# Performance work log

Measured on AMD Instinct MI355X. Metric: run time of the kernel, lower is better.

## Reference

```python
import jax, jax.numpy as jnp
import numpy as np

P = 16          # patch_len
EPS = 1e-5      # BatchNorm eps


def _dct_mats(L):
    # torch_dct DCT-II matrices. Do: norm='ortho' (orthonormal). D2: norm=None (2*cos).
    n = np.arange(L)
    C = np.cos(np.pi * (n[None, :] + 0.5) * n[:, None] / L)
    s = np.full(L, np.sqrt(2.0 / L)); s[0] = np.sqrt(1.0 / L)
    Do = (s[:, None] * C).astype(np.float32)
    D2 = (2.0 * C).astype(np.float32)
    S = np.full(L, 1.0 / np.sqrt(2.0 * L)); S[0] = 1.0 / (2.0 * np.sqrt(L))
    return jnp.asarray(Do), jnp.asarray(D2), jnp.asarray(S.astype(np.float32))


def _gelu(t):
    return jax.nn.gelu(t, approximate=False)


def _bn(x, g, b, ch_axis=1):
    # training-mode BatchNorm1d: biased batch stats over all axes except channel
    axes = tuple(i for i in range(x.ndim) if i != ch_axis)
    m = x.mean(axes, keepdims=True)
    v = ((x - m) ** 2).mean(axes, keepdims=True)
    shp = [1] * x.ndim; shp[ch_axis] = x.shape[ch_axis]
    return (x - m) / jnp.sqrt(v + EPS) * g.reshape(shp) + b.reshape(shp)


def _quantile(a, q):
    # torch.quantile default 'linear' interpolation over flattened tensor
    s = jnp.sort(a)
    n = a.shape[0]
    pos = q * (n - 1)
    lo = jnp.clip(jnp.floor(pos).astype(jnp.int32), 0, n - 1)
    hi = jnp.clip(lo + 1, 0, n - 1)
    frac = pos - lo.astype(pos.dtype)
    return s[lo] * (1.0 - frac) + s[hi] * frac


def _topk_freq(x, Do5, wf, bf, g, b, wc, bc):
    # TopKFreq: first 5 ortho-DCT coeffs per var (torch detaches via cpu/numpy round trip)
    low = jax.lax.stop_gradient(jnp.einsum('bdl,kl->bdk', x, Do5))  # [B,D,5]
    att = jnp.einsum('bdk,k->bd', low, wf) + bf                      # conv1d k=5 stride=5
    m = att.mean(); v = ((att - m) ** 2).mean()                      # BatchNorm1d(1)
    att = (att - m) / jnp.sqrt(v + EPS) * g + b
    att = _gelu(att)
    a = jax.nn.sigmoid(att * wc + bc)                                # 1x1 conv + sigmoid
    return a[:, :, None]  # [B,D,1]; att1 == att2 (same conv used twice)


def _forward(x, dctconv_w, dctconv_b, dctnorm_g, dctnorm_b, threshold,
             embed_W, embed_b, linres_W, linres_b, depth1_w, depth1_b,
             depthnorm_g, depthnorm_b, tf_fc_w, tf_fc_b, tf_norm_g, tf_norm_b,
             tf_conv_w, tf_conv_b, mlp_w1, mlp_b1, mlp_w2, mlp_b2,
             mlpnorm_g, mlpnorm_b):
    B, L, D = x.shape
    N = L // P
    Do, D2, S = _dct_mats(L)
    dctconv = lambda t: t * dctconv_w[None, :, None] + dctconv_b[None, :, None]

    xp = x.transpose(0, 2, 1)                      # [B,D,L]
    x_res = dctconv(xp)
    z_dct = xp @ D2.T                              # dct, norm=None

    # adaptive high-freq mask (rows of 0/1 per (b,d))
    energy = (z_dct ** 2).sum(-1)                  # [B,D]
    med = jnp.median(energy, axis=1, keepdims=True)
    ne = energy / (med + 1e-6)
    thr = _quantile(ne.ravel(), threshold[0])
    mask = (ne > thr).astype(x.dtype)[:, :, None]

    z = dctconv(z_dct * mask)
    z = _gelu(z)
    z = _bn(z, dctnorm_g, dctnorm_b)
    z1 = (z * S) @ Do + x_res                      # idct(norm=None)

    # non-overlapping patching (stride == patch_len)
    zp = xp.reshape(B * D, N, P)
    ze = jnp.einsum('bnp,dp->bnd', zp, embed_W) + embed_b    # [BD,N,3P]
    z_res = ze.reshape(B, D, N * 3 * P) @ linres_W.T + linres_b  # [B,D,pred]

    zr = ze.reshape(B * D, N, P, 3)                # depthwise conv k=3 stride=3
    z1r = jnp.einsum('bnpj,nj->bnp', zr, depth1_w) + depth1_b[None, :, None]
    zd = _gelu(_bn(z1r, depthnorm_g, depthnorm_b))
    z2 = zd.reshape(B, D, L)

    tf = lambda t: _topk_freq(t, Do[:5], tf_fc_w, tf_fc_b[0], tf_norm_g[0],
                              tf_norm_b[0], tf_conv_w[0], tf_conv_b[0])
    att = tf(z1 + z2)
    z1 = z1 * att
    z2 = z2 * att
    z = z1 + z2
    z_att = tf(z)
    z = _gelu(_bn(z, dctnorm_g, dctnorm_b))
    inter = _gelu(_bn(dctconv(z), dctnorm_g, dctnorm_b)) * z_att
    z1 = z1 * inter + z2
    z2 = z2 * inter + z1                           # uses updated z1
    z = z1 * z2 + z1 + z2
    z = _gelu(_bn(z, dctnorm_g, dctnorm_b))

    # Mlp: fc1 applied twice (identical), gelu gate, BN over vars channel, fc2
    h = z @ mlp_w1.T + mlp_b1                      # [B,D,pred//2]
    h = _gelu(h) * h
    h = _bn(h, mlpnorm_g, mlpnorm_b)
    z_mlp = h @ mlp_w2.T + mlp_b2 + z_res          # [B,D,pred]
    return z_mlp.transpose(0, 2, 1)                # [B,pred,D]


def setup_inputs():
    key = jax.random.key(0)
    ks = jax.random.split(key, 14)
    B, L, D, PRED = 2048, 512, 7, 96
    N, DM, H = L // P, 3 * P, PRED // 2
    f32 = jnp.float32
    rn = lambda k, shape, s: jax.random.normal(k, shape, dtype=f32) * s
    return {
        'x': jax.random.normal(ks[0], (B, L, D), dtype=f32),
        'dctconv_w': rn(ks[1], (D,), 0.5),
        'dctconv_b': rn(ks[2], (D,), 0.02),
        'dctnorm_g': jnp.ones((D,), f32),
        'dctnorm_b': jnp.zeros((D,), f32),
        'threshold': jax.random.uniform(ks[3], (1,), dtype=f32) * 0.5,
        'embed_W': rn(ks[4], (DM, P), 0.1),
        'embed_b': rn(ks[5], (DM,), 0.02),
        'linres_W': rn(ks[6], (PRED, N * DM), 0.02),
        'linres_b': rn(ks[7], (PRED,), 0.02),
        'depth1_w': rn(ks[8], (N, 3), 0.3),
        'depth1_b': rn(ks[9], (N,), 0.02),
        'depthnorm_g': jnp.ones((N,), f32),
        'depthnorm_b': jnp.zeros((N,), f32),
        'tf_fc_w': rn(ks[10], (5,), 0.3),
        'tf_fc_b': rn(ks[10], (1,), 0.02),
        'tf_norm_g': jnp.ones((1,), f32),
        'tf_norm_b': jnp.zeros((1,), f32),
        'tf_conv_w': rn(ks[11], (1,), 0.5),
        'tf_conv_b': rn(ks[11], (1,), 0.02),
        'mlp_w1': rn(ks[12], (H, L), 0.04),
        'mlp_b1': rn(ks[12], (H,), 0.02),
        'mlp_w2': rn(ks[13], (PRED, H), 0.1),
        'mlp_b2': rn(ks[13], (PRED,), 0.02),
        'mlpnorm_g': jnp.ones((D,), f32),
        'mlpnorm_b': jnp.zeros((D,), f32),
    }


def reference(x, dctconv_w, dctconv_b, dctnorm_g, dctnorm_b, threshold,
              embed_W, embed_b, linres_W, linres_b, depth1_w, depth1_b,
              depthnorm_g, depthnorm_b, tf_fc_w, tf_fc_b, tf_norm_g, tf_norm_b,
              tf_conv_w, tf_conv_b, mlp_w1, mlp_b1, mlp_w2, mlp_b2,
              mlpnorm_g, mlpnorm_b):
    return _forward(x, dctconv_w, dctconv_b, dctnorm_g, dctnorm_b, threshold,
                    embed_W, embed_b, linres_W, linres_b, depth1_w, depth1_b,
                    depthnorm_g, depthnorm_b, tf_fc_w, tf_fc_b, tf_norm_g,
                    tf_norm_b, tf_conv_w, tf_conv_b, mlp_w1, mlp_b1, mlp_w2,
                    mlp_b2, mlpnorm_g, mlpnorm_b)
```

## Files before the change

kernel.cpp:

```cpp
#include <hip/hip_runtime.h>
#include <math.h>

#define BB 2048
#define LL 512
#define DD 7
#define BD 14336

constexpr size_t F_XP   = 0;
constexpr size_t F_ZG   = F_XP  + (size_t)BD*512;
constexpr size_t F_Z1   = F_ZG  + (size_t)BD*512;
constexpr size_t F_CLK  = F_Z1  + (size_t)BD*512;
constexpr size_t F_MKL  = F_CLK + 512*512;
constexpr size_t F_U    = F_MKL + 512*512;
constexpr size_t F_CSUM = F_U + 512;
constexpr size_t F_W2   = F_CSUM + 512;
constexpr size_t F_CST  = F_W2 + 96*512;
constexpr size_t F_V    = F_CST + 96;
constexpr size_t F_C2   = F_V + 32*256;
constexpr size_t F_ZRES = F_C2 + 512;
constexpr size_t F_H2   = F_ZRES + (size_t)BD*96;
constexpr size_t F_EN   = F_H2 + (size_t)BD*48;
constexpr size_t F_NE   = F_EN + BD;
constexpr size_t F_ATT  = F_NE + BD;
constexpr size_t F_A1   = F_ATT + BD;
constexpr size_t F_A2   = F_A1 + BD;
constexpr size_t F_RS   = F_A2 + BD;
constexpr size_t F_RQ   = F_RS + BD;
constexpr size_t F_PS   = F_RQ + BD;
constexpr size_t F_PQ   = F_PS + 1792*32;
constexpr size_t F_BN   = F_PQ + 1792*32;
constexpr size_t F_THR  = F_BN + 256;

typedef __attribute__((ext_vector_type(8))) short bf8;
typedef __attribute__((ext_vector_type(4))) short sh4;
typedef __attribute__((ext_vector_type(4))) float f4;

__device__ __forceinline__ float gelu_f(float x) {
  return 0.5f * x * (1.0f + erff(x * 0.70710678118654752440f));
}
__device__ __forceinline__ float sigm_f(float x) {
  return 1.0f / (1.0f + expf(-x));
}
__device__ __forceinline__ float wred(float v) {
#pragma unroll
  for (int o = 32; o > 0; o >>= 1) v += __shfl_down(v, o);
  return v;
}
__device__ __forceinline__ unsigned bfh_u(float v) {
  unsigned u = __float_as_uint(v);
  return (u + 0x7FFFu + ((u >> 16) & 1u)) >> 16;
}
__device__ __forceinline__ float bf2f(unsigned h) { return __uint_as_float(h << 16); }

__global__ void k_gen_b(ushort* __restrict__ B1H, ushort* __restrict__ B1L,
                        ushort* __restrict__ B2H, ushort* __restrict__ B2L) {
  int c = blockIdx.x;
  for (int r = threadIdx.x; r < 512; r += 256) {
    double c1 = cos(3.14159265358979323846 * (r + 0.5) * c / 512.0);
    float v1 = (float)(2.0 * c1);
    unsigned h = bfh_u(v1);
    B1H[(size_t)c*512 + r] = (ushort)h;
    B1L[(size_t)c*512 + r] = (ushort)bfh_u(v1 - bf2f(h));
    double c2 = cos(3.14159265358979323846 * (c + 0.5) * r / 512.0);
    float v2 = (float)(c2 * (r == 0 ? (1.0/1024.0) : (1.0/512.0)));
    h = bfh_u(v2);
    B2H[(size_t)c*512 + r] = (ushort)h;
    B2L[(size_t)c*512 + r] = (ushort)bfh_u(v2 - bf2f(h));
  }
}

__global__ void k_ucsum2(float* __restrict__ u, float* __restrict__ csum,
                         const float* __restrict__ wf) {
  int l = blockIdx.x*256 + threadIdx.x;
  if (l >= 512) return;
  double th2 = 3.14159265358979323846 * (double)(2*l + 1) / 2048.0;
  double s = (l & 1) ? -1.0 : 1.0;
  double S = 0.5*s/tan(th2) - 0.5;
  csum[l] = (float)(1.0/1024.0 + S/512.0);
  double uu = (double)wf[0] * 45.25483399593904156 / 1024.0;
  for (int k = 1; k < 5; ++k)
    uu += (double)wf[k] * 32.0 * cos(3.14159265358979323846*(l+0.5)*k/512.0) / 512.0;
  u[l] = (float)uu;
}

__global__ __launch_bounds__(256) void k_w2(const float* __restrict__ linW,
    const float* __restrict__ linb, const float* __restrict__ eW, const float* __restrict__ eb,
    ushort* __restrict__ W2H, ushort* __restrict__ W2L, float* __restrict__ cst)
{
  __shared__ float sW[768];
  __shared__ float sb[48];
  __shared__ float rbuf[256];
  int o = blockIdx.x, t = threadIdx.x;
  for (int i = t; i < 768; i += 256) sW[i] = eW[i];
  if (t < 48) sb[t] = eb[t];
  __syncthreads();
  const float* lw = linW + (size_t)o * 1536;
  for (int i = t; i < 512; i += 256) {
    int n = i >> 4, p = i & 15;
    float s = 0.f;
    const float* l2 = lw + n*48;
#pragma unroll 8
    for (int m = 0; m < 48; ++m) s += l2[m] * sW[m*16 + p];
    unsigned hb = bfh_u(s);
    W2H[(size_t)o*512 + i] = (ushort)hb;
    W2L[(size_t)o*512 + i] = (ushort)bfh_u(s - bf2f(hb));
  }
  float c = 0.f;
  for (int i = t; i < 1536; i += 256) c += lw[i] * sb[i % 48];
  rbuf[t] = c; __syncthreads();
  for (int off = 128; off > 0; off >>= 1) { if (t < off) rbuf[t] += rbuf[t+off]; __syncthreads(); }
  if (t == 0) cst[o] = rbuf[0] + linb[o];
}

__global__ void k_splitw(const float* __restrict__ src, ushort* __restrict__ H,
                         ushort* __restrict__ L, int n) {
  int i = blockIdx.x*256 + threadIdx.x;
  if (i < n) {
    float v = src[i];
    unsigned hb = bfh_u(v);
    H[i] = (ushort)hb;
    L[i] = (ushort)bfh_u(v - bf2f(hb));
  }
}

__global__ void k_v(const float* __restrict__ eW, const float* __restrict__ eb,
                    const float* __restrict__ dw, const float* __restrict__ db,
                    float* __restrict__ V, float* __restrict__ c2)
{
  int n = blockIdx.x, t = threadIdx.x;
  int p = t >> 4, q = t & 15;
  float s = 0.f;
#pragma unroll
  for (int j = 0; j < 3; ++j) s += eW[(p*3+j)*16 + q] * dw[n*3+j];
  V[(size_t)n*256 + p*16 + q] = s;
  if (q == 0) {
    float c = 0.f;
#pragma unroll
    for (int j = 0; j < 3; ++j) c += eb[p*3+j] * dw[n*3+j];
    c2[n*16+p] = c + db[n];
  }
}

__global__ __launch_bounds__(256) void k_transpose(const float* __restrict__ x,
                                                   float* __restrict__ xp,
                                                   float* __restrict__ en) {
  __shared__ float s[3584];
  int b = blockIdx.x;
  const float* src = x + (size_t)b*3584;
  for (int c = threadIdx.x; c < 896; c += 256) {
    float4 v = *(const float4*)&src[c*4];
    s[c*4+0]=v.x; s[c*4+1]=v.y; s[c*4+2]=v.z; s[c*4+3]=v.w;
  }
  __syncthreads();
  for (int c = threadIdx.x; c < 896; c += 256) {
    int d = c >> 7, cg = c & 127;
    float4 v;
    v.x = s[(cg*4+0)*7 + d]; v.y = s[(cg*4+1)*7 + d];
    v.z = s[(cg*4+2)*7 + d]; v.w = s[(cg*4+3)*7 + d];
    *(float4*)&xp[((size_t)b*7 + d)*512 + cg*4] = v;
  }
  int t = threadIdx.x;
  if (t < 224) {
    int d = t >> 5, c0 = (t & 31) * 16;
    double ss = 0.0, qq = 0.0;
    for (int l = c0; l < c0 + 16; ++l) {
      double v = s[l*7 + d];
      ss += v; qq += v*v;
    }
#pragma unroll
    for (int o = 16; o > 0; o >>= 1) {
      ss += __shfl_down(ss, o, 32);
      qq += __shfl_down(qq, o, 32);
    }
    if ((t & 31) == 0) en[b*7 + d] = (float)(1024.0*qq + 2.0*ss*ss);
  }
}

template<int MODE>
__global__ __launch_bounds__(512) void k_mfma(
    const float* __restrict__ Af32,
    const ushort* __restrict__ AHg, const ushort* __restrict__ ALg,
    const ushort* __restrict__ BHg, const ushort* __restrict__ BLg,
    float* __restrict__ z1out, ushort* __restrict__ GH, ushort* __restrict__ GL,
    const float* __restrict__ bnac, const float* __restrict__ csum,
    const float* __restrict__ xp,
    const float* __restrict__ cw, const float* __restrict__ cb,
    const float* __restrict__ ne, const float* __restrict__ thr,
    float* __restrict__ rs, float* __restrict__ rq)
{
  __shared__ ushort AhS[64*40], AlS[64*40];
  __shared__ ushort BhS[256*40], BlS[256*40];
  const int t = threadIdx.x;
  const int lane = t & 63, w = t >> 6;
  const int l15 = lane & 15, l4 = lane >> 4;
  const int rg = w & 1, cg = w >> 1;
  const int r0 = blockIdx.x * 64, c0 = blockIdx.y * 256;

  f4 acc[2][4];
#pragma unroll
  for (int i = 0; i < 2; ++i)
#pragma unroll
    for (int j = 0; j < 4; ++j) acc[i][j] = (f4){0.f,0.f,0.f,0.f};

  const int arow = t >> 3, ak0 = (t & 7) * 4;

  for (int kt = 0; kt < 512; kt += 32) {
    if (MODE == 2) {
      const float* src = Af32 + (size_t)(r0+arow)*512 + kt + ak0;
      float4 v0 = *(const float4*)src;
      float va[4] = {v0.x,v0.y,v0.z,v0.w};
      sh4 hv, lv;
#pragma unroll
      for (int j = 0; j < 4; ++j) {
        unsigned hb = bfh_u(va[j]);
        hv[j] = (short)hb;
        lv[j] = (short)bfh_u(va[j] - bf2f(hb));
      }
      *(sh4*)&AhS[arow*40 + ak0] = hv;
      *(sh4*)&AlS[arow*40 + ak0] = lv;
    } else {
      *(sh4*)&AhS[arow*40 + ak0] = *(const sh4*)&AHg[(size_t)(r0+arow)*512 + kt + ak0];
      *(sh4*)&AlS[arow*40 + ak0] = *(const sh4*)&ALg[(size_t)(r0+arow)*512 + kt + ak0];
    }
#pragma unroll
    for (int h = 0; h < 2; ++h) {
      int c = t + h*512;
      int brow = c >> 2, bk0 = (c & 3) * 8;
      *(bf8*)&BhS[brow*40 + bk0] = *(const bf8*)&BHg[(size_t)(c0+brow)*512 + kt + bk0];
      *(bf8*)&BlS[brow*40 + bk0] = *(const bf8*)&BLg[(size_t)(c0+brow)*512 + kt + bk0];
    }
    __syncthreads();
    bf8 ah[2], al[2], bh[4], bl[4];
#pragma unroll
    for (int fr = 0; fr < 2; ++fr) {
      int off = (rg*32 + fr*16 + l15)*40 + l4*8;
      ah[fr] = *(const bf8*)&AhS[off];
      al[fr] = *(const bf8*)&AlS[off];
    }
#pragma unroll
    for (int fc = 0; fc < 4; ++fc) {
      int off = (cg*64 + fc*16 + l15)*40 + l4*8;
      bh[fc] = *(const bf8*)&BhS[off];
      bl[fc] = *(const bf8*)&BlS[off];
    }
#pragma unroll
    for (int fr = 0; fr < 2; ++fr)
#pragma unroll
      for (int fc = 0; fc < 4; ++fc) {
        acc[fr][fc] = __builtin_amdgcn_mfma_f32_16x16x32_bf16(ah[fr], bh[fc], acc[fr][fc], 0, 0, 0);
        acc[fr][fc] = __builtin_amdgcn_mfma_f32_16x16x32_bf16(ah[fr], bl[fc], acc[fr][fc], 0, 0, 0);
        acc[fr][fc] = __builtin_amdgcn_mfma_f32_16x16x32_bf16(al[fr], bh[fc], acc[fr][fc], 0, 0, 0);
      }
    __syncthreads();
  }

  const float thv = (MODE == 2) ? thr[0] : 0.f;
#pragma unroll
  for (int fr = 0; fr < 2; ++fr)
#pragma unroll
    for (int j = 0; j < 4; ++j) {
      const int r = r0 + rg*32 + fr*16 + l4*4 + j;
      const int d = r % 7;
      if (MODE == 1) {
        const float aR = bnac[d], cR = bnac[7+d], wv = cw[d], bvv = cb[d];
#pragma unroll
        for (int fc = 0; fc < 4; ++fc) {
          int col = c0 + cg*64 + fc*16 + l15;
          float val = acc[fr][fc][j];
          z1out[(size_t)r*512 + col] = aR*val + cR*csum[col] + xp[(size_t)r*512 + col]*wv + bvv;
        }
      } else {
        float m = (ne[r] > thv) ? 1.0f : 0.0f;
        float wm = cw[d] * m, bvv = cb[d];
        float s = 0.f, q = 0.f;
#pragma unroll
        for (int fc = 0; fc < 4; ++fc) {
          int col = c0 + cg*64 + fc*16 + l15;
          float g = gelu_f(acc[fr][fc][j]*wm + bvv);
          unsigned hb = bfh_u(g);
          GH[(size_t)r*512 + col] = (ushort)hb;
          GL[(size_t)r*512 + col] = (ushort)bfh_u(g - bf2f(hb));
          s += g; q += g*g;
        }
#pragma unroll
        for (int off = 8; off > 0; off >>= 1) {
          s += __shfl_down(s, off, 16);
          q += __shfl_down(q, off, 16);
        }
        if (l15 == 0) { atomicAdd(&rs[r], s); atomicAdd(&rq[r], q); }
      }
    }
}

template<int NCOLS, int MODE>
__global__ __launch_bounds__(256) void k_mfma_nt(
    const float* __restrict__ Af32,
    const ushort* __restrict__ WH, const ushort* __restrict__ WL,
    const float* __restrict__ bias, float* __restrict__ outp,
    const float* __restrict__ ta, const float* __restrict__ tc,
    float* __restrict__ rs, float* __restrict__ rq)
{
  constexpr int NF = NCOLS / 16;
  __shared__ ushort AhS[64*40], AlS[64*40];
  __shared__ ushort BhS[NCOLS*40], BlS[NCOLS*40];
  const int t = threadIdx.x;
  const int lane = t & 63, w = t >> 6;
  const int l15 = lane & 15, l4 = lane >> 4;
  const int r0 = blockIdx.x * 64;

  f4 acc[NF];
#pragma unroll
  for (int fc = 0; fc < NF; ++fc) acc[fc] = (f4){0.f,0.f,0.f,0.f};

  const int arow = t >> 2, ak0 = (t & 3) * 8;
  float taa = 0.f, tcc = 0.f;
  if (MODE == 1) { int d = (r0 + arow) % 7; taa = ta[d]; tcc = tc[d]; }

  for (int kt = 0; kt < 512; kt += 32) {
    {
      const float* src = Af32 + (size_t)(r0+arow)*512 + kt + ak0;
      float4 v0 = *(const float4*)src;
      float4 v1 = *(const float4*)(src+4);
      float va[8] = {v0.x,v0.y,v0.z,v0.w,v1.x,v1.y,v1.z,v1.w};
      bf8 hv, lv;
#pragma unroll
      for (int j = 0; j < 8; ++j) {
        float x = va[j];
        if (MODE == 1) x = gelu_f(taa*x + tcc);
        unsigned hb = bfh_u(x);
        hv[j] = (short)hb;
        lv[j] = (short)bfh_u(x - bf2f(hb));
      }
      *(bf8*)&AhS[arow*40 + ak0] = hv;
      *(bf8*)&AlS[arow*40 + ak0] = lv;
    }
    for (int c = t; c < NCOLS*4; c += 256) {
      int brow = c >> 2, bk0 = (c & 3) * 8;
      *(bf8*)&BhS[brow*40 + bk0] = *(const bf8*)&WH[(size_t)brow*512 + kt + bk0];
      *(bf8*)&BlS[brow*40 + bk0] = *(const bf8*)&WL[(size_t)brow*512 + kt + bk0];
    }
    __syncthreads();
    bf8 ah, al;
    {
      int off = (w*16 + l15)*40 + l4*8;
      ah = *(const bf8*)&AhS[off];
      al = *(const bf8*)&AlS[off];
    }
#pragma unroll
    for (int fc = 0; fc < NF; ++fc) {
      int off = (fc*16 + l15)*40 + l4*8;
      bf8 bh = *(const bf8*)&BhS[off];
      bf8 bl = *(const bf8*)&BlS[off];
      acc[fc] = __builtin_amdgcn_mfma_f32_16x16x32_bf16(ah, bh, acc[fc], 0, 0, 0);
      acc[fc] = __builtin_amdgcn_mfma_f32_16x16x32_bf16(ah, bl, acc[fc], 0, 0, 0);
      acc[fc] = __builtin_amdgcn_mfma_f32_16x16x32_bf16(al, bh, acc[fc], 0, 0, 0);
    }
    __syncthreads();
  }

#pragma unroll
  for (int j = 0; j < 4; ++j) {
    const int r = r0 + w*16 + l4*4 + j;
    float s = 0.f, q = 0.f;
#pragma unroll
    for (int fc = 0; fc < NF; ++fc) {
      int col = fc*16 + l15;
      float v = acc[fc][j] + bias[col];
      if (MODE == 1) { float g = gelu_f(v); v = g*v; }
      outp[(size_t)r*NCOLS + col] = v;
      if (MODE == 1) { s += v; q += v*v; }
    }
    if (MODE == 1) {
#pragma unroll
      for (int off = 8; off > 0; off >>= 1) {
        s += __shfl_down(s, off, 16);
        q += __shfl_down(q, off, 16);
      }
      if (l15 == 0) { rs[r] = s; rq[r] = q; }
    }
  }
}

__global__ void k_ne(const float* __restrict__ en, float* __restrict__ ne) {
  int b = blockIdx.x*256 + threadIdx.x;
  if (b >= 2048) return;
  float e[7], s7[7];
#pragma unroll
  for (int d = 0; d < 7; ++d) { e[d] = en[b*7+d]; s7[d] = e[d]; }
#pragma unroll
  for (int i = 1; i < 7; ++i) {
    float key = s7[i]; int j = i-1;
    while (j >= 0 && s7[j] > key) { s7[j+1] = s7[j]; --j; }
    s7[j+1] = key;
  }
  float med = s7[3] + 1e-6f;
#pragma unroll
  for (int d = 0; d < 7; ++d) ne[b*7+d] = e[d] / med;
}

__global__ __launch_bounds__(1024) void k_thr(const float* __restrict__ ne,
                                              const float* __restrict__ qp, float* __restrict__ out)
{
  __shared__ unsigned s_part[16][8];
  __shared__ unsigned s_bsel, s_R;
  const int t = threadIdx.x;
  const int lane = t & 63, wv = t >> 6;
  unsigned key[14];
#pragma unroll
  for (int j = 0; j < 14; ++j) key[j] = __float_as_uint(ne[t + j*1024]);

  float q = qp[0];
  float pos = q * 14335.0f;
  int lo = (int)floorf(pos);
  if (lo < 0) lo = 0; if (lo > 14335) lo = 14335;
  int hi = lo + 1; if (hi > 14335) hi = 14335;
  float frac = pos - (float)lo;

  unsigned prefix = 0;
  unsigned R = (unsigned)lo;
#pragma unroll 1
  for (int shift = 28; shift >= 0; shift -= 4) {
    unsigned pb = prefix >> shift;
    unsigned long long accb = 0ull;
#pragma unroll
    for (int j = 0; j < 14; ++j) {
      unsigned diff = (key[j] >> shift) - pb;
      accb += (diff < 16u) ? (1ull << (diff*4)) : 0ull;
    }
    unsigned pk[8];
#pragma unroll
    for (int b = 0; b < 8; ++b) {
      unsigned clo = (unsigned)(accb >> (b*4)) & 15u;
      unsigned chi = (unsigned)(accb >> (b*4+32)) & 15u;
      pk[b] = clo | (chi << 16);
    }
#pragma unroll
    for (int b = 0; b < 8; ++b)
#pragma unroll
      for (int o = 32; o > 0; o >>= 1) pk[b] += __shfl_down(pk[b], o);
    if (lane == 0) {
#pragma unroll
      for (int b = 0; b < 8; ++b) s_part[wv][b] = pk[b];
    }
    __syncthreads();
    if (t == 0) {
      unsigned tot[16];
#pragma unroll
      for (int i = 0; i < 8; ++i) {
        unsigned s = 0;
#pragma unroll
        for (int w2 = 0; w2 < 16; ++w2) s += s_part[w2][i];
        tot[i] = s & 0xFFFFu; tot[i+8] = s >> 16;
      }
      unsigned cum = 0, bsel = 15;
#pragma unroll 1
      for (int b = 0; b < 16; ++b) {
        if (cum + tot[b] > R) { bsel = (unsigned)b; break; }
        cum += tot[b];
      }
      s_bsel = bsel; s_R = R - cum;
    }
    __syncthreads();
    prefix |= (s_bsel << shift);
    R = s_R;
    __syncthreads();
  }
  unsigned cle = 0, mn = 0xFFFFFFFFu;
#pragma unroll
  for (int j = 0; j < 14; ++j) {
    cle += (key[j] <= prefix) ? 1u : 0u;
    if (key[j] > prefix && key[j] < mn) mn = key[j];
  }
#pragma unroll
  for (int o = 32; o > 0; o >>= 1) {
    cle += __shfl_down(cle, o);
    unsigned m2 = __shfl_down(mn, o);
    mn = (m2 < mn) ? m2 : mn;
  }
  if (lane == 0) { s_part[wv][0] = cle; s_part[wv][1] = mn; }
  __syncthreads();
  if (t == 0) {
    unsigned C = 0, M = 0xFFFFFFFFu;
#pragma unroll
    for (int w2 = 0; w2 < 16; ++w2) {
      C += s_part[w2][0];
      if (s_part[w2][1] < M) M = s_part[w2][1];
    }
    unsigned vhiKey = (C > (unsigned)hi) ? prefix : M;
    if (vhiKey == 0xFFFFFFFFu) vhiKey = prefix;
    float vlo = __uint_as_float(prefix);
    float vhi = __uint_as_float(vhiKey);
    out[0] = vlo*(1.0f-frac) + vhi*frac;
  }
}

__global__ __launch_bounds__(256) void k_bnfin_rows(const float* __restrict__ rs,
    const float* __restrict__ rq, int nch, int nrows, double count,
    const float* __restrict__ gamma, const float* __restrict__ beta, float* __restrict__ out)
{
  __shared__ double sd[256];
  int ch = blockIdx.x, t = threadIdx.x;
  double s = 0.0, q = 0.0;
  for (int i = ch + t*nch; i < nrows; i += 256*nch) { s += rs[i]; q += rq[i]; }
  sd[t] = s; __syncthreads();
  for (int o = 128; o > 0; o >>= 1) { if (t < o) sd[t] += sd[t+o]; __syncthreads(); }
  double S = sd[0]; __syncthreads();
  sd[t] = q; __syncthreads();
  for (int o = 128; o > 0; o >>= 1) { if (t < o) sd[t] += sd[t+o]; __syncthreads(); }
  if (t == 0) {
    double m = S / count;
    double v = sd[0] / count - m*m; if (v < 0.0) v = 0.0;
    double inv = 1.0 / sqrt(v + 1e-5);
    out[ch]       = (float)(gamma[ch] * inv);
    out[nch + ch] = (float)(beta[ch] - m * gamma[ch] * inv);
  }
}

__global__ __launch_bounds__(256) void k_bnfin_part(const float* __restrict__ pS,
    const float* __restrict__ pQ, int nparts, int nch, double count,
    const float* __restrict__ gamma, const float* __restrict__ beta, float* __restrict__ out)
{
  __shared__ double sd[256];
  int ch = blockIdx.x, t = threadIdx.x;
  double s = 0.0, q = 0.0;
  for (int i = t; i < nparts; i += 256) { s += pS[(size_t)i*nch + ch]; q += pQ[(size_t)i*nch + ch]; }
  sd[t] = s; __syncthreads();
  for (int o = 128; o > 0; o >>= 1) { if (t < o) sd[t] += sd[t+o]; __syncthreads(); }
  double S = sd[0]; __syncthreads();
  sd[t] = q; __syncthreads();
  for (int o = 128; o > 0; o >>= 1) { if (t < o) sd[t] += sd[t+o]; __syncthreads(); }
  if (t == 0) {
    double m = S / count;
    double v = sd[0] / count - m*m; if (v < 0.0) v = 0.0;
    double inv = 1.0 / sqrt(v + 1e-5);
    out[ch]       = (float)(gamma[ch] * inv);
    out[nch + ch] = (float)(beta[ch] - m * gamma[ch] * inv);
  }
}

__global__ __launch_bounds__(256) void k_patch(const float* __restrict__ xp,
    const float* __restrict__ V, const float* __restrict__ c2,
    float* __restrict__ z1r, float* __restrict__ pS, float* __restrict__ pQ)
{
  __shared__ float sx[8][512];
  __shared__ float aS[32], aQ[32];
  int t = threadIdx.x;
  int r0 = blockIdx.x * 8;
  for (int c = t; c < 1024; c += 256) {
    int row = c >> 7, cg = c & 127;
    *(float4*)&sx[row][cg*4] = *(const float4*)&xp[(size_t)(r0+row)*512 + cg*4];
  }
  if (t < 32) { aS[t] = 0.f; aQ[t] = 0.f; }
  __syncthreads();
  float vreg[2][16]; float cc[2]; int nn_[2], oo[2];
#pragma unroll
  for (int h = 0; h < 2; ++h) {
    int o = t + h*256;
    oo[h] = o;
    int n = o >> 4, p = o & 15;
    nn_[h] = n;
#pragma unroll
    for (int qg = 0; qg < 4; ++qg) {
      float4 v4 = *(const float4*)&V[(size_t)n*256 + p*16 + qg*4];
      vreg[h][qg*4+0]=v4.x; vreg[h][qg*4+1]=v4.y; vreg[h][qg*4+2]=v4.z; vreg[h][qg*4+3]=v4.w;
    }
    cc[h] = c2[o];
  }
  float sum[2] = {0.f,0.f}, sq[2] = {0.f,0.f};
  for (int row = 0; row < 8; ++row) {
#pragma unroll
    for (int h = 0; h < 2; ++h) {
      const float* xr = &sx[row][nn_[h]*16];
      float val = cc[h];
#pragma unroll
      for (int qq = 0; qq < 16; ++qq) val += vreg[h][qq] * xr[qq];
      z1r[(size_t)(r0+row)*512 + oo[h]] = val;
      sum[h] += val; sq[h] += val*val;
    }
  }
#pragma unroll
  for (int h = 0; h < 2; ++h) {
    atomicAdd(&aS[nn_[h]], sum[h]);
    atomicAdd(&aQ[nn_[h]], sq[h]);
  }
  __syncthreads();
  if (t < 32) { pS[(size_t)blockIdx.x*32 + t] = aS[t]; pQ[(size_t)blockIdx.x*32 + t] = aQ[t]; }
}

__global__ void k_att(const float* __restrict__ z1, const float* __restrict__ z1r,
    const float* __restrict__ bn2, const float* __restrict__ u, const float* __restrict__ fcb,
    float* __restrict__ att)
{
  int r = blockIdx.x*4 + (threadIdx.x >> 6);
  int lane = threadIdx.x & 63;
  const float* z1p = z1 + (size_t)r*512;
  const float* zrp = z1r + (size_t)r*512;
  float s = 0.f;
#pragma unroll
  for (int h = 0; h < 2; ++h) {
    int i = lane*4 + h*256;
    int n = i >> 4;
    float a2n = bn2[n], c2n = bn2[32+n];
    float4 zr = *(const float4*)&zrp[i];
    float4 zv = *(const float4*)&z1p[i];
    float4 uv = *(const float4*)&u[i];
    s += (zv.x + gelu_f(a2n*zr.x + c2n)) * uv.x;
    s += (zv.y + gelu_f(a2n*zr.y + c2n)) * uv.y;
    s += (zv.z + gelu_f(a2n*zr.z + c2n)) * uv.z;
    s += (zv.w + gelu_f(a2n*zr.w + c2n)) * uv.w;
  }
  s = wred(s);
  if (lane == 0) att[r] = s + fcb[0];
}

__global__ __launch_bounds__(1024) void k_tf(const float* __restrict__ att,
    const float* __restrict__ pg, const float* __restrict__ pb,
    const float* __restrict__ pwc, const float* __restrict__ pbc,
    const float* __restrict__ pfb, float* __restrict__ a1, float* __restrict__ a2)
{
  __shared__ double sd[1024];
  __shared__ float sh[4];
  const int t = threadIdx.x;
  float g = pg[0], b = pb[0], wc = pwc[0], bc = pbc[0], fb = pfb[0];
  double s = 0.0, q = 0.0;
  for (int i = t; i < BD; i += 1024) { double v = att[i]; s += v; q += v*v; }
  sd[t] = s; __syncthreads();
  for (int o = 512; o > 0; o >>= 1) { if (t < o) sd[t] += sd[t+o]; __syncthreads(); }
  double S1 = sd[0]; __syncthreads();
  sd[t] = q; __syncthreads();
  for (int o = 512; o > 0; o >>= 1) { if (t < o) sd[t] += sd[t+o]; __syncthreads(); }
  if (t == 0) {
    double m = S1 / 14336.0;
    double v = sd[0] / 14336.0 - m*m; if (v < 0.0) v = 0.0;
    sh[0] = (float)m; sh[1] = (float)(1.0 / sqrt(v + 1e-5));
  }
  __syncthreads();
  float m1 = sh[0], i1 = sh[1];
  s = 0.0; q = 0.0;
  for (int i = t; i < BD; i += 1024) {
    float v = att[i];
    float an = (v - m1) * i1 * g + b;
    float av = sigm_f(gelu_f(an) * wc + bc);
    a1[i] = av;
    float t2 = av * (v - fb) + fb;
    s += t2; q += (double)t2 * t2;
  }
  __syncthreads();
  sd[t] = s; __syncthreads();
  for (int o = 512; o > 0; o >>= 1) { if (t < o) sd[t] += sd[t+o]; __syncthreads(); }
  double S2 = sd[0]; __syncthreads();
  sd[t] = q; __syncthreads();
  for (int o = 512; o > 0; o >>= 1) { if (t < o) sd[t] += sd[t+o]; __syncthreads(); }
  if (t == 0) {
    double m = S2 / 14336.0;
    double v = sd[0] / 14336.0 - m*m; if (v < 0.0) v = 0.0;
    sh[2] = (float)m; sh[3] = (float)(1.0 / sqrt(v + 1e-5));
  }
  __syncthreads();
  float m2 = sh[2], i2 = sh[3];
  for (int i = t; i < BD; i += 1024) {
    float t2 = a1[i] * (att[i] - fb) + fb;
    float an = (t2 - m2) * i2 * g + b;
    a2[i] = sigm_f(gelu_f(an) * wc + bc);
  }
}

__global__ void k_statsA(const float* __restrict__ z1, const float* __restrict__ z1r,
    const float* __restrict__ bn2, const float* __restrict__ a1,
    float* __restrict__ rs, float* __restrict__ rq)
{
  int r = blockIdx.x*4 + (threadIdx.x >> 6);
  int lane = threadIdx.x & 63;
  float av = a1[r];
  const float* z1p = z1 + (size_t)r*512;
  const float* zrp = z1r + (size_t)r*512;
  float s = 0.f, q = 0.f;
#pragma unroll
  for (int h = 0; h < 2; ++h) {
    int i = lane*4 + h*256;
    int n = i >> 4;
    float a2n = bn2[n], c2n = bn2[32+n];
    float4 zr = *(const float4*)&zrp[i];
    float4 zv = *(const float4*)&z1p[i];
    float A0 = (zv.x + gelu_f(a2n*zr.x + c2n)) * av;
    float A1 = (zv.y + gelu_f(a2n*zr.y + c2n)) * av;
    float A2 = (zv.z + gelu_f(a2n*zr.z + c2n)) * av;
    float A3 = (zv.w + gelu_f(a2n*zr.w + c2n)) * av;
    s += A0+A1+A2+A3; q += A0*A0+A1*A1+A2*A2+A3*A3;
  }
  s = wred(s); q = wred(q);
  if (lane == 0) { rs[r] = s; rq[r] = q; }
}

__global__ void k_statsC(const float* __restrict__ z1, const float* __restrict__ z1r,
    const float* __restrict__ bn2, const float* __restrict__ a1,
    const float* __restrict__ bn3, const float* __restrict__ cw, const float* __restrict__ cb,
    float* __restrict__ rs, float* __restrict__ rq)
{
  int r = blockIdx.x*4 + (threadIdx.x >> 6);
  int lane = threadIdx.x & 63;
  int d = r % 7;
  float av = a1[r];
  float b3a = bn3[d], b3c = bn3[7+d], wv = cw[d], bv = cb[d];
  const float* z1p = z1 + (size_t)r*512;
  const float* zrp = z1r + (size_t)r*512;
  float s = 0.f, q = 0.f;
#pragma unroll
  for (int h = 0; h < 2; ++h) {
    int i = lane*4 + h*256;
    int n = i >> 4;
    float a2n = bn2[n], c2n = bn2[32+n];
    float4 zr = *(const float4*)&zrp[i];
    float4 zv = *(const float4*)&z1p[i];
#pragma unroll
    for (int e = 0; e < 4; ++e) {
      float ze = (e==0?zr.x:e==1?zr.y:e==2?zr.z:zr.w);
      float z1e = (e==0?zv.x:e==1?zv.y:e==2?zv.z:zv.w);
      float A = (z1e + gelu_f(a2n*ze + c2n)) * av;
      float C = wv*gelu_f(b3a*A + b3c) + bv;
      s += C; q += C*C;
    }
  }
  s = wred(s); q = wred(q);
  if (lane == 0) { rs[r] = s; rq[r] = q; }
}

__global__ void k_final(const float* __restrict__ z1, const float* __restrict__ z1r,
    const float* __restrict__ bn2, const float* __restrict__ a1, const float* __restrict__ a2,
    const float* __restrict__ bn3, const float* __restrict__ bn4,
    const float* __restrict__ cw, const float* __restrict__ cb,
    float* __restrict__ zf, float* __restrict__ rs, float* __restrict__ rq)
{
  int r = blockIdx.x*4 + (threadIdx.x >> 6);
  int lane = threadIdx.x & 63;
  int d = r % 7;
  float av = a1[r], a2v = a2[r];
  float b3a = bn3[d], b3c = bn3[7+d], b4a = bn4[d], b4c = bn4[7+d];
  float wv = cw[d], bv = cb[d];
  const float* z1p = z1 + (size_t)r*512;
  const float* zrp = z1r + (size_t)r*512;
  float* zfp = zf + (size_t)r*512;
  float s = 0.f, q = 0.f;
#pragma unroll
  for (int h = 0; h < 2; ++h) {
    int i = lane*4 + h*256;
    int n = i >> 4;
    float a2n = bn2[n], c2n = bn2[32+n];
    float4 zr = *(const float4*)&zrp[i];
    float4 zv = *(const float4*)&z1p[i];
    float4 ov;
#pragma unroll
    for (int e = 0; e < 4; ++e) {
      float ze = (e==0?zr.x:e==1?zr.y:e==2?zr.z:zr.w);
      float z1e = (e==0?zv.x:e==1?zv.y:e==2?zv.z:zv.w);
      float z1v = z1e * av;
      float z2v = gelu_f(a2n*ze + c2n) * av;
      float A = z1v + z2v;
      float C = wv*gelu_f(b3a*A + b3c) + bv;
      float inter = gelu_f(b4a*C + b4c) * a2v;
      float z1n = z1v*inter + z2v;
      float z2n = z2v*inter + z1n;
      float zfv = z1n*z2n + z1n + z2n;
      (e==0?ov.x:e==1?ov.y:e==2?ov.z:ov.w) = zfv;
      s += zfv; q += zfv*zfv;
    }
    *(float4*)&zfp[i] = ov;
  }
  s = wred(s); q = wred(q);
  if (lane == 0) { rs[r] = s; rq[r] = q; }
}

__global__ __launch_bounds__(256) void k_out(const float* __restrict__ h2,
    const float* __restrict__ bn6, const float* __restrict__ w2, const float* __restrict__ b2,
    const float* __restrict__ zres, float* __restrict__ out)
{
  int idx = blockIdx.x*256 + threadIdx.x;
  int r = idx / 96, o = idx - r*96;
  int d = r % 7, b = r / 7;
  float a6 = bn6[d], c6 = bn6[7+d];
  const float* hp = h2 + (size_t)r*48;
  const float* wp = w2 + o*48;
  float s = 0.f;
#pragma unroll
  for (int j4 = 0; j4 < 12; ++j4) {
    float4 hv = *(const float4*)&hp[j4*4];
    float4 wv = *(const float4*)&wp[j4*4];
    s += (a6*hv.x + c6)*wv.x + (a6*hv.y + c6)*wv.y
       + (a6*hv.z + c6)*wv.z + (a6*hv.w + c6)*wv.w;
  }
  out[(size_t)b*672 + o*7 + d] = s + b2[o] + zres[(size_t)r*96 + o];
}

extern "C" void kernel_launch(void* const* d_in, const int* in_sizes, int n_in,
                              void* d_out, int out_size, void* d_ws, size_t ws_size,
                              hipStream_t stream) {
  const float* x          = (const float*)d_in[0];
  const float* dctconv_w  = (const float*)d_in[1];
  const float* dctconv_b  = (const float*)d_in[2];
  const float* dctnorm_g  = (const float*)d_in[3];
  const float* dctnorm_b  = (const float*)d_in[4];
  const float* threshold  = (const float*)d_in[5];
  const float* embed_W    = (const float*)d_in[6];
  const float* embed_b    = (const float*)d_in[7];
  const float* linres_W   = (const float*)d_in[8];
  const float* linres_b   = (const float*)d_in[9];
  const float* depth1_w   = (const float*)d_in[10];
  const float* depth1_b   = (const float*)d_in[11];
  const float* depthnorm_g= (const float*)d_in[12];
  const float* depthnorm_b= (const float*)d_in[13];
  const float* tf_fc_w    = (const float*)d_in[14];
  const float* tf_fc_b    = (const float*)d_in[15];
  const float* tf_norm_g  = (const float*)d_in[16];
  const float* tf_norm_b  = (const float*)d_in[17];
  const float* tf_conv_w  = (const float*)d_in[18];
  const float* tf_conv_b  = (const float*)d_in[19];
  const float* mlp_w1     = (const float*)d_in[20];
  const float* mlp_b1     = (const float*)d_in[21];
  const float* mlp_w2     = (const float*)d_in[22];
  const float* mlp_b2     = (const float*)d_in[23];
  const float* mlpnorm_g  = (const float*)d_in[24];
  const float* mlpnorm_b  = (const float*)d_in[25];
  float* out = (float*)d_out;
  float* ws  = (float*)d_ws;

  float* XP   = ws + F_XP;
  float* ZG   = ws + F_ZG;
  ushort* ZGH = (ushort*)(ws + F_ZG);
  ushort* ZGL = ZGH + (size_t)BD*512;
  float* Z1   = ws + F_Z1;
  ushort* B1H = (ushort*)(ws + F_CLK);
  ushort* B1L = B1H + 512*512;
  ushort* W2H = (ushort*)(ws + F_CLK + 131072);
  ushort* W2L = W2H + 96*512;
  ushort* W1H = W2L + 96*512;
  ushort* W1L = W1H + 48*512;
  ushort* B2H = (ushort*)(ws + F_MKL);
  ushort* B2L = B2H + 512*512;
  float* U    = ws + F_U;
  float* CSUM = ws + F_CSUM;
  float* CSTp = ws + F_CST;
  float* Vp   = ws + F_V;
  float* C2p  = ws + F_C2;
  float* ZRES = ws + F_ZRES;
  float* H2p  = ws + F_H2;
  float* EN   = ws + F_EN;
  float* NEp  = ws + F_NE;
  float* ATTp = ws + F_ATT;
  float* A1p  = ws + F_A1;
  float* A2p  = ws + F_A2;
  float* RS   = ws + F_RS;
  float* RQ   = ws + F_RQ;
  float* PS   = ws + F_PS;
  float* PQ   = ws + F_PQ;
  float* BN0  = ws + F_BN;
  float* BN2  = ws + F_BN + 16;
  float* BN3  = ws + F_BN + 80;
  float* BN4  = ws + F_BN + 96;
  float* BN5  = ws + F_BN + 112;
  float* BN6  = ws + F_BN + 128;
  float* THRp = ws + F_THR;

  k_gen_b<<<512, 256, 0, stream>>>(B1H, B1L, B2H, B2L);
  k_ucsum2<<<2, 256, 0, stream>>>(U, CSUM, tf_fc_w);
  k_w2<<<96, 256, 0, stream>>>(linres_W, linres_b, embed_W, embed_b, W2H, W2L, CSTp);
  k_splitw<<<96, 256, 0, stream>>>(mlp_w1, W1H, W1L, 48*512);
  k_v<<<32, 256, 0, stream>>>(embed_W, embed_b, depth1_w, depth1_b, Vp, C2p);
  k_transpose<<<2048, 256, 0, stream>>>(x, XP, EN);
  k_ne<<<8, 256, 0, stream>>>(EN, NEp);
  k_thr<<<1, 1024, 0, stream>>>(NEp, threshold, THRp);
  hipMemsetAsync(RS, 0, 2*BD*sizeof(float), stream);
  k_mfma<2><<<dim3(224,2), 512, 0, stream>>>(XP, nullptr, nullptr, B1H, B1L,
      nullptr, ZGH, ZGL, nullptr, nullptr, nullptr, dctconv_w, dctconv_b,
      NEp, THRp, RS, RQ);
  k_bnfin_rows<<<7, 256, 0, stream>>>(RS, RQ, 7, BD, 1048576.0, dctnorm_g, dctnorm_b, BN0);
  k_mfma<1><<<dim3(224,2), 512, 0, stream>>>(nullptr, ZGH, ZGL, B2H, B2L,
      Z1, nullptr, nullptr, BN0, CSUM, XP, dctconv_w, dctconv_b,
      nullptr, nullptr, nullptr, nullptr);
  k_patch<<<1792, 256, 0, stream>>>(XP, Vp, C2p, ZG, PS, PQ);
  k_bnfin_part<<<32, 256, 0, stream>>>(PS, PQ, 1792, 32, 229376.0, depthnorm_g, depthnorm_b, BN2);
  k_mfma_nt<96,0><<<224, 256, 0, stream>>>(XP, W2H, W2L, CSTp, ZRES,
      nullptr, nullptr, nullptr, nullptr);
  k_att<<<3584, 256, 0, stream>>>(Z1, ZG, BN2, U, tf_fc_b, ATTp);
  k_tf<<<1, 1024, 0, stream>>>(ATTp, tf_norm_g, tf_norm_b, tf_conv_w, tf_conv_b, tf_fc_b, A1p, A2p);
  k_statsA<<<3584, 256, 0, stream>>>(Z1, ZG, BN2, A1p, RS, RQ);
  k_bnfin_rows<<<7, 256, 0, stream>>>(RS, RQ, 7, BD, 1048576.0, dctnorm_g, dctnorm_b, BN3);
  k_statsC<<<3584, 256, 0, stream>>>(Z1, ZG, BN2, A1p, BN3, dctconv_w, dctconv_b, RS, RQ);
  k_bnfin_rows<<<7, 256, 0, stream>>>(RS, RQ, 7, BD, 1048576.0, dctnorm_g, dctnorm_b, BN4);
  k_final<<<3584, 256, 0, stream>>>(Z1, ZG, BN2, A1p, A2p, BN3, BN4, dctconv_w, dctconv_b, XP, RS, RQ);
  k_bnfin_rows<<<7, 256, 0, stream>>>(RS, RQ, 7, BD, 1048576.0, dctnorm_g, dctnorm_b, BN5);
  k_mfma_nt<48,1><<<224, 256, 0, stream>>>(XP, W1H, W1L, mlp_b1, H2p,
      BN5, BN5+7, RS, RQ);
  k_bnfin_rows<<<7, 256, 0, stream>>>(RS, RQ, 7, BD, 98304.0, mlpnorm_g, mlpnorm_b, BN6);
  k_out<<<5376, 256, 0, stream>>>(H2p, BN6, mlp_w2, mlp_b2, ZRES, out);
}
```

Before: 379.8 us.

## Fuse setup kernels, retile DCT GEMMs, drop statsA pass, store final z as bf16 split

```diff
diff --git a/kernel.cpp b/kernel.cpp
--- a/kernel.cpp
+++ b/kernel.cpp
@@ -30,6 +30,7 @@
 constexpr size_t F_PQ   = F_PS + 1792*32;
 constexpr size_t F_BN   = F_PQ + 1792*32;
 constexpr size_t F_THR  = F_BN + 256;
+constexpr size_t F_W1   = F_THR + 16;
 
 typedef __attribute__((ext_vector_type(8))) short bf8;
 typedef __attribute__((ext_vector_type(4))) short sh4;
@@ -52,99 +53,99 @@
 }
 __device__ __forceinline__ float bf2f(unsigned h) { return __uint_as_float(h << 16); }
 
-__global__ void k_gen_b(ushort* __restrict__ B1H, ushort* __restrict__ B1L,
-                        ushort* __restrict__ B2H, ushort* __restrict__ B2L) {
-  int c = blockIdx.x;
-  for (int r = threadIdx.x; r < 512; r += 256) {
-    double c1 = cos(3.14159265358979323846 * (r + 0.5) * c / 512.0);
-    float v1 = (float)(2.0 * c1);
-    unsigned h = bfh_u(v1);
-    B1H[(size_t)c*512 + r] = (ushort)h;
-    B1L[(size_t)c*512 + r] = (ushort)bfh_u(v1 - bf2f(h));
-    double c2 = cos(3.14159265358979323846 * (c + 0.5) * r / 512.0);
-    float v2 = (float)(c2 * (r == 0 ? (1.0/1024.0) : (1.0/512.0)));
-    h = bfh_u(v2);
-    B2H[(size_t)c*512 + r] = (ushort)h;
-    B2L[(size_t)c*512 + r] = (ushort)bfh_u(v2 - bf2f(h));
-  }
-}
-
-__global__ void k_ucsum2(float* __restrict__ u, float* __restrict__ csum,
-                         const float* __restrict__ wf) {
-  int l = blockIdx.x*256 + threadIdx.x;
-  if (l >= 512) return;
-  double th2 = 3.14159265358979323846 * (double)(2*l + 1) / 2048.0;
-  double s = (l & 1) ? -1.0 : 1.0;
-  double S = 0.5*s/tan(th2) - 0.5;
-  csum[l] = (float)(1.0/1024.0 + S/512.0);
-  double uu = (double)wf[0] * 45.25483399593904156 / 1024.0;
-  for (int k = 1; k < 5; ++k)
-    uu += (double)wf[k] * 32.0 * cos(3.14159265358979323846*(l+0.5)*k/512.0) / 512.0;
-  u[l] = (float)uu;
-}
-
-__global__ __launch_bounds__(256) void k_w2(const float* __restrict__ linW,
-    const float* __restrict__ linb, const float* __restrict__ eW, const float* __restrict__ eb,
+#define PI1024 0.00306796157577128218f
+
+__global__ __launch_bounds__(256) void k_setup(
+    ushort* __restrict__ B1H, ushort* __restrict__ B1L,
+    ushort* __restrict__ B2H, ushort* __restrict__ B2L,
+    float* __restrict__ u, float* __restrict__ csum, const float* __restrict__ wf,
+    const float* __restrict__ eW, const float* __restrict__ eb,
+    const float* __restrict__ dw, const float* __restrict__ db,
+    float* __restrict__ V, float* __restrict__ c2,
+    const float* __restrict__ mlpw1, ushort* __restrict__ W1H, ushort* __restrict__ W1L,
+    const float* __restrict__ linW, const float* __restrict__ linb,
     ushort* __restrict__ W2H, ushort* __restrict__ W2L, float* __restrict__ cst)
 {
   __shared__ float sW[768];
   __shared__ float sb[48];
   __shared__ float rbuf[256];
-  int o = blockIdx.x, t = threadIdx.x;
-  for (int i = t; i < 768; i += 256) sW[i] = eW[i];
-  if (t < 48) sb[t] = eb[t];
-  __syncthreads();
-  const float* lw = linW + (size_t)o * 1536;
-  for (int i = t; i < 512; i += 256) {
-    int n = i >> 4, p = i & 15;
+  const int bid = blockIdx.x, t = threadIdx.x;
+  if (bid < 512) {
+    int c = bid;
+    for (int r = t; r < 512; r += 256) {
+      int n1 = ((2*r + 1) * c) & 2047;
+      float v1 = 2.0f * cosf((float)n1 * PI1024);
+      unsigned h = bfh_u(v1);
+      B1H[(size_t)c*512 + r] = (ushort)h;
+      B1L[(size_t)c*512 + r] = (ushort)bfh_u(v1 - bf2f(h));
+      int n2 = ((2*c + 1) * r) & 2047;
+      float v2 = cosf((float)n2 * PI1024) * (r == 0 ? (1.0f/1024.0f) : (1.0f/512.0f));
+      h = bfh_u(v2);
+      B2H[(size_t)c*512 + r] = (ushort)h;
+      B2L[(size_t)c*512 + r] = (ushort)bfh_u(v2 - bf2f(h));
+    }
+  } else if (bid < 514) {
+    int l = (bid - 512)*256 + t;
+    if (l < 512) {
+      double th2 = 3.14159265358979323846 * (double)(2*l + 1) / 2048.0;
+      double s = (l & 1) ? -1.0 : 1.0;
+      double S = 0.5*s/tan(th2) - 0.5;
+      csum[l] = (float)(1.0/1024.0 + S/512.0);
+      double uu = (double)wf[0] * 45.25483399593904156 / 1024.0;
+      for (int k = 1; k < 5; ++k)
+        uu += (double)wf[k] * 32.0 * cos(3.14159265358979323846*(l+0.5)*k/512.0) / 512.0;
+      u[l] = (float)uu;
+    }
+  } else if (bid < 546) {
+    int n = bid - 514;
+    int p = t >> 4, q = t & 15;
     float s = 0.f;
-    const float* l2 = lw + n*48;
+#pragma unroll
+    for (int j = 0; j < 3; ++j) s += eW[(p*3+j)*16 + q] * dw[n*3+j];
+    V[(size_t)n*256 + p*16 + q] = s;
+    if (q == 0) {
+      float c = 0.f;
+#pragma unroll
+      for (int j = 0; j < 3; ++j) c += eb[p*3+j] * dw[n*3+j];
+      c2[n*16+p] = c + db[n];
+    }
+  } else if (bid < 642) {
+    int i = (bid - 546)*256 + t;
+    if (i < 48*512) {
+      float v = mlpw1[i];
+      unsigned hb = bfh_u(v);
+      W1H[i] = (ushort)hb;
+      W1L[i] = (ushort)bfh_u(v - bf2f(hb));
+    }
+  } else {
+    int o = bid - 642;
+    for (int i = t; i < 768; i += 256) sW[i] = eW[i];
+    if (t < 48) sb[t] = eb[t];
+    __syncthreads();
+    const float* lw = linW + (size_t)o * 1536;
+    for (int i = t; i < 512; i += 256) {
+      int n = i >> 4, p = i & 15;
+      float s = 0.f;
+      const float* l2 = lw + n*48;
 #pragma unroll 8
-    for (int m = 0; m < 48; ++m) s += l2[m] * sW[m*16 + p];
-    unsigned hb = bfh_u(s);
-    W2H[(size_t)o*512 + i] = (ushort)hb;
-    W2L[(size_t)o*512 + i] = (ushort)bfh_u(s - bf2f(hb));
-  }
-  float c = 0.f;
-  for (int i = t; i < 1536; i += 256) c += lw[i] * sb[i % 48];
-  rbuf[t] = c; __syncthreads();
-  for (int off = 128; off > 0; off >>= 1) { if (t < off) rbuf[t] += rbuf[t+off]; __syncthreads(); }
-  if (t == 0) cst[o] = rbuf[0] + linb[o];
-}
-
-__global__ void k_splitw(const float* __restrict__ src, ushort* __restrict__ H,
-                         ushort* __restrict__ L, int n) {
-  int i = blockIdx.x*256 + threadIdx.x;
-  if (i < n) {
-    float v = src[i];
-    unsigned hb = bfh_u(v);
-    H[i] = (ushort)hb;
-    L[i] = (ushort)bfh_u(v - bf2f(hb));
-  }
-}
-
-__global__ void k_v(const float* __restrict__ eW, const float* __restrict__ eb,
-                    const float* __restrict__ dw, const float* __restrict__ db,
-                    float* __restrict__ V, float* __restrict__ c2)
-{
-  int n = blockIdx.x, t = threadIdx.x;
-  int p = t >> 4, q = t & 15;
-  float s = 0.f;
-#pragma unroll
-  for (int j = 0; j < 3; ++j) s += eW[(p*3+j)*16 + q] * dw[n*3+j];
-  V[(size_t)n*256 + p*16 + q] = s;
-  if (q == 0) {
+      for (int m = 0; m < 48; ++m) s += l2[m] * sW[m*16 + p];
+      unsigned hb = bfh_u(s);
+      W2H[(size_t)o*512 + i] = (ushort)hb;
+      W2L[(size_t)o*512 + i] = (ushort)bfh_u(s - bf2f(hb));
+    }
     float c = 0.f;
-#pragma unroll
-    for (int j = 0; j < 3; ++j) c += eb[p*3+j] * dw[n*3+j];
-    c2[n*16+p] = c + db[n];
+    for (int i = t; i < 1536; i += 256) c += lw[i] * sb[i % 48];
+    rbuf[t] = c; __syncthreads();
+    for (int off = 128; off > 0; off >>= 1) { if (t < off) rbuf[t] += rbuf[t+off]; __syncthreads(); }
+    if (t == 0) cst[o] = rbuf[0] + linb[o];
   }
 }
 
 __global__ __launch_bounds__(256) void k_transpose(const float* __restrict__ x,
                                                    float* __restrict__ xp,
-                                                   float* __restrict__ en) {
+                                                   float* __restrict__ ne) {
   __shared__ float s[3584];
+  __shared__ float sEn[7];
   int b = blockIdx.x;
   const float* src = x + (size_t)b*3584;
   for (int c = threadIdx.x; c < 896; c += 256) {
@@ -172,12 +173,27 @@
       ss += __shfl_down(ss, o, 32);
       qq += __shfl_down(qq, o, 32);
     }
-    if ((t & 31) == 0) en[b*7 + d] = (float)(1024.0*qq + 2.0*ss*ss);
+    if ((t & 31) == 0) sEn[d] = (float)(1024.0*qq + 2.0*ss*ss);
+  }
+  __syncthreads();
+  if (t == 0) {
+    float e[7], s7[7];
+#pragma unroll
+    for (int d = 0; d < 7; ++d) { e[d] = sEn[d]; s7[d] = e[d]; }
+#pragma unroll
+    for (int i = 1; i < 7; ++i) {
+      float key = s7[i]; int j = i-1;
+      while (j >= 0 && s7[j] > key) { s7[j+1] = s7[j]; --j; }
+      s7[j+1] = key;
+    }
+    float med = s7[3] + 1e-6f;
+#pragma unroll
+    for (int d = 0; d < 7; ++d) ne[b*7 + d] = e[d] / med;
   }
 }
 
 template<int MODE>
-__global__ __launch_bounds__(512) void k_mfma(
+__global__ __launch_bounds__(256) void k_mfma(
     const float* __restrict__ Af32,
     const ushort* __restrict__ AHg, const ushort* __restrict__ ALg,
     const ushort* __restrict__ BHg, const ushort* __restrict__ BLg,
@@ -188,63 +204,68 @@
     const float* __restrict__ ne, const float* __restrict__ thr,
     float* __restrict__ rs, float* __restrict__ rq)
 {
-  __shared__ ushort AhS[64*40], AlS[64*40];
-  __shared__ ushort BhS[256*40], BlS[256*40];
+  __shared__ ushort AhS[128*40], AlS[128*40];
+  __shared__ ushort BhS[128*40], BlS[128*40];
   const int t = threadIdx.x;
   const int lane = t & 63, w = t >> 6;
   const int l15 = lane & 15, l4 = lane >> 4;
-  const int rg = w & 1, cg = w >> 1;
-  const int r0 = blockIdx.x * 64, c0 = blockIdx.y * 256;
-
-  f4 acc[2][4];
-#pragma unroll
-  for (int i = 0; i < 2; ++i)
+  const int wr = (w & 1)*64, wc = (w >> 1)*64;
+  const int r0 = blockIdx.x * 128, c0 = blockIdx.y * 128;
+
+  f4 acc[4][4];
+#pragma unroll
+  for (int i = 0; i < 4; ++i)
 #pragma unroll
     for (int j = 0; j < 4; ++j) acc[i][j] = (f4){0.f,0.f,0.f,0.f};
 
-  const int arow = t >> 3, ak0 = (t & 7) * 4;
+  const int arow = t >> 1, ak0 = (t & 1) * 16;
 
   for (int kt = 0; kt < 512; kt += 32) {
     if (MODE == 2) {
-      const float* src = Af32 + (size_t)(r0+arow)*512 + kt + ak0;
-      float4 v0 = *(const float4*)src;
-      float va[4] = {v0.x,v0.y,v0.z,v0.w};
-      sh4 hv, lv;
-#pragma unroll
-      for (int j = 0; j < 4; ++j) {
-        unsigned hb = bfh_u(va[j]);
-        hv[j] = (short)hb;
-        lv[j] = (short)bfh_u(va[j] - bf2f(hb));
+#pragma unroll
+      for (int g = 0; g < 2; ++g) {
+        const float* src = Af32 + (size_t)(r0+arow)*512 + kt + ak0 + g*8;
+        float4 v0 = *(const float4*)src;
+        float4 v1 = *(const float4*)(src+4);
+        float va[8] = {v0.x,v0.y,v0.z,v0.w,v1.x,v1.y,v1.z,v1.w};
+        bf8 hv, lv;
+#pragma unroll
+        for (int j = 0; j < 8; ++j) {
+          unsigned hb = bfh_u(va[j]);
+          hv[j] = (short)hb;
+          lv[j] = (short)bfh_u(va[j] - bf2f(hb));
+        }
+        *(bf8*)&AhS[arow*40 + ak0 + g*8] = hv;
+        *(bf8*)&AlS[arow*40 + ak0 + g*8] = lv;
       }
-      *(sh4*)&AhS[arow*40 + ak0] = hv;
-      *(sh4*)&AlS[arow*40 + ak0] = lv;
     } else {
-      *(sh4*)&AhS[arow*40 + ak0] = *(const sh4*)&AHg[(size_t)(r0+arow)*512 + kt + ak0];
-      *(sh4*)&AlS[arow*40 + ak0] = *(const sh4*)&ALg[(size_t)(r0+arow)*512 + kt + ak0];
-    }
-#pragma unroll
-    for (int h = 0; h < 2; ++h) {
-      int c = t + h*512;
-      int brow = c >> 2, bk0 = (c & 3) * 8;
-      *(bf8*)&BhS[brow*40 + bk0] = *(const bf8*)&BHg[(size_t)(c0+brow)*512 + kt + bk0];
-      *(bf8*)&BlS[brow*40 + bk0] = *(const bf8*)&BLg[(size_t)(c0+brow)*512 + kt + bk0];
+#pragma unroll
+      for (int g = 0; g < 2; ++g) {
+        *(bf8*)&AhS[arow*40 + ak0 + g*8] = *(const bf8*)&AHg[(size_t)(r0+arow)*512 + kt + ak0 + g*8];
+        *(bf8*)&AlS[arow*40 + ak0 + g*8] = *(const bf8*)&ALg[(size_t)(r0+arow)*512 + kt + ak0 + g*8];
+      }
+    }
+#pragma unroll
+    for (int g = 0; g < 2; ++g) {
+      *(bf8*)&BhS[arow*40 + ak0 + g*8] = *(const bf8*)&BHg[(size_t)(c0+arow)*512 + kt + ak0 + g*8];
+      *(bf8*)&BlS[arow*40 + ak0 + g*8] = *(const bf8*)&BLg[(size_t)(c0+arow)*512 + kt + ak0 + g*8];
     }
     __syncthreads();
-    bf8 ah[2], al[2], bh[4], bl[4];
-#pragma unroll
-    for (int fr = 0; fr < 2; ++fr) {
-      int off = (rg*32 + fr*16 + l15)*40 + l4*8;
+    bf8 ah[4], al[4], bh[4], bl[4];
+#pragma unroll
+    for (int fr = 0; fr < 4; ++fr) {
+      int off = (wr + fr*16 + l15)*40 + l4*8;
       ah[fr] = *(const bf8*)&AhS[off];
       al[fr] = *(const bf8*)&AlS[off];
     }
 #pragma unroll
     for (int fc = 0; fc < 4; ++fc) {
-      int off = (cg*64 + fc*16 + l15)*40 + l4*8;
+      int off = (wc + fc*16 + l15)*40 + l4*8;
       bh[fc] = *(const bf8*)&BhS[off];
       bl[fc] = *(const bf8*)&BlS[off];
     }
 #pragma unroll
-    for (int fr = 0; fr < 2; ++fr)
+    for (int fr = 0; fr < 4; ++fr)
 #pragma unroll
       for (int fc = 0; fc < 4; ++fc) {
         acc[fr][fc] = __builtin_amdgcn_mfma_f32_16x16x32_bf16(ah[fr], bh[fc], acc[fr][fc], 0, 0, 0);
@@ -256,16 +277,16 @@
 
   const float thv = (MODE == 2) ? thr[0] : 0.f;
 #pragma unroll
-  for (int fr = 0; fr < 2; ++fr)
+  for (int fr = 0; fr < 4; ++fr)
 #pragma unroll
     for (int j = 0; j < 4; ++j) {
-      const int r = r0 + rg*32 + fr*16 + l4*4 + j;
+      const int r = r0 + wr + fr*16 + l4*4 + j;
       const int d = r % 7;
       if (MODE == 1) {
         const float aR = bnac[d], cR = bnac[7+d], wv = cw[d], bvv = cb[d];
 #pragma unroll
         for (int fc = 0; fc < 4; ++fc) {
-          int col = c0 + cg*64 + fc*16 + l15;
+          int col = c0 + wc + fc*16 + l15;
           float val = acc[fr][fc][j];
           z1out[(size_t)r*512 + col] = aR*val + cR*csum[col] + xp[(size_t)r*512 + col]*wv + bvv;
         }
@@ -275,7 +296,7 @@
         float s = 0.f, q = 0.f;
 #pragma unroll
         for (int fc = 0; fc < 4; ++fc) {
-          int col = c0 + cg*64 + fc*16 + l15;
+          int col = c0 + wc + fc*16 + l15;
           float g = gelu_f(acc[fr][fc][j]*wm + bvv);
           unsigned hb = bfh_u(g);
           GH[(size_t)r*512 + col] = (ushort)hb;
@@ -295,6 +316,7 @@
 template<int NCOLS, int MODE>
 __global__ __launch_bounds__(256) void k_mfma_nt(
     const float* __restrict__ Af32,
+    const ushort* __restrict__ AHp, const ushort* __restrict__ ALp,
     const ushort* __restrict__ WH, const ushort* __restrict__ WL,
     const float* __restrict__ bias, float* __restrict__ outp,
     const float* __restrict__ ta, const float* __restrict__ tc,
@@ -314,22 +336,32 @@
 
   const int arow = t >> 2, ak0 = (t & 3) * 8;
   float taa = 0.f, tcc = 0.f;
-  if (MODE == 1) { int d = (r0 + arow) % 7; taa = ta[d]; tcc = tc[d]; }
+  if (MODE == 2) { int d = (r0 + arow) % 7; taa = ta[d]; tcc = tc[d]; }
 
   for (int kt = 0; kt < 512; kt += 32) {
     {
-      const float* src = Af32 + (size_t)(r0+arow)*512 + kt + ak0;
-      float4 v0 = *(const float4*)src;
-      float4 v1 = *(const float4*)(src+4);
-      float va[8] = {v0.x,v0.y,v0.z,v0.w,v1.x,v1.y,v1.z,v1.w};
+      float va[8];
+      if (MODE == 0) {
+        const float* src = Af32 + (size_t)(r0+arow)*512 + kt + ak0;
+        float4 v0 = *(const float4*)src;
+        float4 v1 = *(const float4*)(src+4);
+        va[0]=v0.x; va[1]=v0.y; va[2]=v0.z; va[3]=v0.w;
+        va[4]=v1.x; va[5]=v1.y; va[6]=v1.z; va[7]=v1.w;
+      } else {
+        bf8 hv8 = *(const bf8*)&AHp[(size_t)(r0+arow)*512 + kt + ak0];
+        bf8 lv8 = *(const bf8*)&ALp[(size_t)(r0+arow)*512 + kt + ak0];
+#pragma unroll
+        for (int j = 0; j < 8; ++j) {
+          float xv = bf2f((unsigned)(ushort)hv8[j]) + bf2f((unsigned)(ushort)lv8[j]);
+          va[j] = gelu_f(taa*xv + tcc);
+        }
+      }
       bf8 hv, lv;
 #pragma unroll
       for (int j = 0; j < 8; ++j) {
-        float x = va[j];
-        if (MODE == 1) x = gelu_f(taa*x + tcc);
-        unsigned hb = bfh_u(x);
+        unsigned hb = bfh_u(va[j]);
         hv[j] = (short)hb;
-        lv[j] = (short)bfh_u(x - bf2f(hb));
+        lv[j] = (short)bfh_u(va[j] - bf2f(hb));
       }
       *(bf8*)&AhS[arow*40 + ak0] = hv;
       *(bf8*)&AlS[arow*40 + ak0] = lv;
@@ -366,11 +398,11 @@
     for (int fc = 0; fc < NF; ++fc) {
       int col = fc*16 + l15;
       float v = acc[fc][j] + bias[col];
-      if (MODE == 1) { float g = gelu_f(v); v = g*v; }
+      if (MODE == 2) { float g = gelu_f(v); v = g*v; }
       outp[(size_t)r*NCOLS + col] = v;
-      if (MODE == 1) { s += v; q += v*v; }
-    }
-    if (MODE == 1) {
+      if (MODE == 2) { s += v; q += v*v; }
+    }
+    if (MODE == 2) {
 #pragma unroll
       for (int off = 8; off > 0; off >>= 1) {
         s += __shfl_down(s, off, 16);
@@ -379,23 +411,6 @@
       if (l15 == 0) { rs[r] = s; rq[r] = q; }
     }
   }
-}
-
-__global__ void k_ne(const float* __restrict__ en, float* __restrict__ ne) {
-  int b = blockIdx.x*256 + threadIdx.x;
-  if (b >= 2048) return;
-  float e[7], s7[7];
-#pragma unroll
-  for (int d = 0; d < 7; ++d) { e[d] = en[b*7+d]; s7[d] = e[d]; }
-#pragma unroll
-  for (int i = 1; i < 7; ++i) {
-    float key = s7[i]; int j = i-1;
-    while (j >= 0 && s7[j] > key) { s7[j+1] = s7[j]; --j; }
-    s7[j+1] = key;
-  }
-  float med = s7[3] + 1e-6f;
-#pragma unroll
-  for (int d = 0; d < 7; ++d) ne[b*7+d] = e[d] / med;
 }
 
 __global__ __launch_bounds__(1024) void k_thr(const float* __restrict__ ne,
@@ -516,6 +531,32 @@
   }
 }
 
+__global__ __launch_bounds__(256) void k_bnfin_scaled(const float* __restrict__ S1,
+    const float* __restrict__ Q1, const float* __restrict__ a1,
+    const float* __restrict__ gamma, const float* __restrict__ beta, float* __restrict__ out)
+{
+  __shared__ double sd[256];
+  int ch = blockIdx.x, t = threadIdx.x;
+  double s = 0.0, q = 0.0;
+  for (int i = ch + t*7; i < BD; i += 256*7) {
+    double a = a1[i];
+    s += a * S1[i];
+    q += a*a * Q1[i];
+  }
+  sd[t] = s; __syncthreads();
+  for (int o = 128; o > 0; o >>= 1) { if (t < o) sd[t] += sd[t+o]; __syncthreads(); }
+  double S = sd[0]; __syncthreads();
+  sd[t] = q; __syncthreads();
+  for (int o = 128; o > 0; o >>= 1) { if (t < o) sd[t] += sd[t+o]; __syncthreads(); }
+  if (t == 0) {
+    double m = S / 1048576.0;
+    double v = sd[0] / 1048576.0 - m*m; if (v < 0.0) v = 0.0;
+    double inv = 1.0 / sqrt(v + 1e-5);
+    out[ch]     = (float)(gamma[ch] * inv);
+    out[7 + ch] = (float)(beta[ch] - m * gamma[ch] * inv);
+  }
+}
+
 __global__ __launch_bounds__(256) void k_bnfin_part(const float* __restrict__ pS,
     const float* __restrict__ pQ, int nparts, int nch, double count,
     const float* __restrict__ gamma, const float* __restrict__ beta, float* __restrict__ out)
@@ -589,13 +630,13 @@
 
 __global__ void k_att(const float* __restrict__ z1, const float* __restrict__ z1r,
     const float* __restrict__ bn2, const float* __restrict__ u, const float* __restrict__ fcb,
-    float* __restrict__ att)
+    float* __restrict__ att, float* __restrict__ S1o, float* __restrict__ Q1o)
 {
   int r = blockIdx.x*4 + (threadIdx.x >> 6);
   int lane = threadIdx.x & 63;
   const float* z1p = z1 + (size_t)r*512;
   const float* zrp = z1r + (size_t)r*512;
-  float s = 0.f;
+  float s = 0.f, s1 = 0.f, q1 = 0.f;
 #pragma unroll
   for (int h = 0; h < 2; ++h) {
     int i = lane*4 + h*256;
@@ -604,13 +645,17 @@
     float4 zr = *(const float4*)&zrp[i];
     float4 zv = *(const float4*)&z1p[i];
     float4 uv = *(const float4*)&u[i];
-    s += (zv.x + gelu_f(a2n*zr.x + c2n)) * uv.x;
-    s += (zv.y + gelu_f(a2n*zr.y + c2n)) * uv.y;
-    s += (zv.z + gelu_f(a2n*zr.z + c2n)) * uv.z;
-    s += (zv.w + gelu_f(a2n*zr.w + c2n)) * uv.w;
-  }
-  s = wred(s);
-  if (lane == 0) att[r] = s + fcb[0];
+#pragma unroll
+    for (int e = 0; e < 4; ++e) {
+      float ze = (e==0?zr.x:e==1?zr.y:e==2?zr.z:zr.w);
+      float z1e = (e==0?zv.x:e==1?zv.y:e==2?zv.z:zv.w);
+      float ue = (e==0?uv.x:e==1?uv.y:e==2?uv.z:uv.w);
+      float tv = z1e + gelu_f(a2n*ze + c2n);
+      s += tv * ue; s1 += tv; q1 += tv*tv;
+    }
+  }
+  s = wred(s); s1 = wred(s1); q1 = wred(q1);
+  if (lane == 0) { att[r] = s + fcb[0]; S1o[r] = s1; Q1o[r] = q1; }
 }
 
 __global__ __launch_bounds__(1024) void k_tf(const float* __restrict__ att,
@@ -665,33 +710,6 @@
   }
 }
 
-__global__ void k_statsA(const float* __restrict__ z1, const float* __restrict__ z1r,
-    const float* __restrict__ bn2, const float* __restrict__ a1,
-    float* __restrict__ rs, float* __restrict__ rq)
-{
-  int r = blockIdx.x*4 + (threadIdx.x >> 6);
-  int lane = threadIdx.x & 63;
-  float av = a1[r];
-  const float* z1p = z1 + (size_t)r*512;
-  const float* zrp = z1r + (size_t)r*512;
-  float s = 0.f, q = 0.f;
-#pragma unroll
-  for (int h = 0; h < 2; ++h) {
-    int i = lane*4 + h*256;
-    int n = i >> 4;
-    float a2n = bn2[n], c2n = bn2[32+n];
-    float4 zr = *(const float4*)&zrp[i];
-    float4 zv = *(const float4*)&z1p[i];
-    float A0 = (zv.x + gelu_f(a2n*zr.x + c2n)) * av;
-    float A1 = (zv.y + gelu_f(a2n*zr.y + c2n)) * av;
-    float A2 = (zv.z + gelu_f(a2n*zr.z + c2n)) * av;
-    float A3 = (zv.w + gelu_f(a2n*zr.w + c2n)) * av;
-    s += A0+A1+A2+A3; q += A0*A0+A1*A1+A2*A2+A3*A3;
-  }
-  s = wred(s); q = wred(q);
-  if (lane == 0) { rs[r] = s; rq[r] = q; }
-}
-
 __global__ void k_statsC(const float* __restrict__ z1, const float* __restrict__ z1r,
     const float* __restrict__ bn2, const float* __restrict__ a1,
     const float* __restrict__ bn3, const float* __restrict__ cw, const float* __restrict__ cb,
@@ -729,7 +747,8 @@
     const float* __restrict__ bn2, const float* __restrict__ a1, const float* __restrict__ a2,
     const float* __restrict__ bn3, const float* __restrict__ bn4,
     const float* __restrict__ cw, const float* __restrict__ cb,
-    float* __restrict__ zf, float* __restrict__ rs, float* __restrict__ rq)
+    ushort* __restrict__ zfh, ushort* __restrict__ zfl,
+    float* __restrict__ rs, float* __restrict__ rq)
 {
   int r = blockIdx.x*4 + (threadIdx.x >> 6);
   int lane = threadIdx.x & 63;
@@ -739,7 +758,6 @@
   float wv = cw[d], bv = cb[d];
   const float* z1p = z1 + (size_t)r*512;
   const float* zrp = z1r + (size_t)r*512;
-  float* zfp = zf + (size_t)r*512;
   float s = 0.f, q = 0.f;
 #pragma unroll
   for (int h = 0; h < 2; ++h) {
@@ -748,7 +766,7 @@
     float a2n = bn2[n], c2n = bn2[32+n];
     float4 zr = *(const float4*)&zrp[i];
     float4 zv = *(const float4*)&z1p[i];
-    float4 ov;
+    sh4 hv, lv;
 #pragma unroll
     for (int e = 0; e < 4; ++e) {
       float ze = (e==0?zr.x:e==1?zr.y:e==2?zr.z:zr.w);
@@ -761,10 +779,13 @@
       float z1n = z1v*inter + z2v;
       float z2n = z2v*inter + z1n;
       float zfv = z1n*z2n + z1n + z2n;
-      (e==0?ov.x:e==1?ov.y:e==2?ov.z:ov.w) = zfv;
+      unsigned hb = bfh_u(zfv);
+      hv[e] = (short)hb;
+      lv[e] = (short)bfh_u(zfv - bf2f(hb));
       s += zfv; q += zfv*zfv;
     }
-    *(float4*)&zfp[i] = ov;
+    *(sh4*)&zfh[(size_t)r*512 + i] = hv;
+    *(sh4*)&zfl[(size_t)r*512 + i] = lv;
   }
   s = wred(s); q = wred(q);
   if (lane == 0) { rs[r] = s; rq[r] = q; }
@@ -824,18 +845,20 @@
   float* ws  = (float*)d_ws;
 
   float* XP   = ws + F_XP;
+  ushort* ZFH = (ushort*)(ws + F_XP);
+  ushort* ZFL = ZFH + (size_t)BD*512;
   float* ZG   = ws + F_ZG;
   ushort* ZGH = (ushort*)(ws + F_ZG);
   ushort* ZGL = ZGH + (size_t)BD*512;
   float* Z1   = ws + F_Z1;
   ushort* B1H = (ushort*)(ws + F_CLK);
   ushort* B1L = B1H + 512*512;
-  ushort* W2H = (ushort*)(ws + F_CLK + 131072);
-  ushort* W2L = W2H + 96*512;
-  ushort* W1H = W2L + 96*512;
-  ushort* W1L = W1H + 48*512;
   ushort* B2H = (ushort*)(ws + F_MKL);
   ushort* B2L = B2H + 512*512;
+  ushort* W2H = (ushort*)(ws + F_W2);
+  ushort* W2L = W2H + 96*512;
+  ushort* W1H = (ushort*)(ws + F_W1);
+  ushort* W1L = W1H + 48*512;
   float* U    = ws + F_U;
   float* CSUM = ws + F_CSUM;
   float* CSTp = ws + F_CST;
@@ -843,7 +866,6 @@
   float* C2p  = ws + F_C2;
   float* ZRES = ws + F_ZRES;
   float* H2p  = ws + F_H2;
-  float* EN   = ws + F_EN;
   float* NEp  = ws + F_NE;
   float* ATTp = ws + F_ATT;
   float* A1p  = ws + F_A1;
@@ -860,35 +882,32 @@
   float* BN6  = ws + F_BN + 128;
   float* THRp = ws + F_THR;
 
-  k_gen_b<<<512, 256, 0, stream>>>(B1H, B1L, B2H, B2L);
-  k_ucsum2<<<2, 256, 0, stream>>>(U, CSUM, tf_fc_w);
-  k_w2<<<96, 256, 0, stream>>>(linres_W, linres_b, embed_W, embed_b, W2H, W2L, CSTp);
-  k_splitw<<<96, 256, 0, stream>>>(mlp_w1, W1H, W1L, 48*512);
-  k_v<<<32, 256, 0, stream>>>(embed_W, embed_b, depth1_w, depth1_b, Vp, C2p);
-  k_transpose<<<2048, 256, 0, stream>>>(x, XP, EN);
-  k_ne<<<8, 256, 0, stream>>>(EN, NEp);
+  k_setup<<<738, 256, 0, stream>>>(B1H, B1L, B2H, B2L, U, CSUM, tf_fc_w,
+      embed_W, embed_b, depth1_w, depth1_b, Vp, C2p,
+      mlp_w1, W1H, W1L, linres_W, linres_b, W2H, W2L, CSTp);
+  k_transpose<<<2048, 256, 0, stream>>>(x, XP, NEp);
   k_thr<<<1, 1024, 0, stream>>>(NEp, threshold, THRp);
   hipMemsetAsync(RS, 0, 2*BD*sizeof(float), stream);
-  k_mfma<2><<<dim3(224,2), 512, 0, stream>>>(XP, nullptr, nullptr, B1H, B1L,
+  k_mfma<2><<<dim3(112,4), 256, 0, stream>>>(XP, nullptr, nullptr, B1H, B1L,
       nullptr, ZGH, ZGL, nullptr, nullptr, nullptr, dctconv_w, dctconv_b,
       NEp, THRp, RS, RQ);
   k_bnfin_rows<<<7, 256, 0, stream>>>(RS, RQ, 7, BD, 1048576.0, dctnorm_g, dctnorm_b, BN0);
-  k_mfma<1><<<dim3(224,2), 512, 0, stream>>>(nullptr, ZGH, ZGL, B2H, B2L,
+  k_mfma<1><<<dim3(112,4), 256, 0, stream>>>(nullptr, ZGH, ZGL, B2H, B2L,
       Z1, nullptr, nullptr, BN0, CSUM, XP, dctconv_w, dctconv_b,
       nullptr, nullptr, nullptr, nullptr);
   k_patch<<<1792, 256, 0, stream>>>(XP, Vp, C2p, ZG, PS, PQ);
   k_bnfin_part<<<32, 256, 0, stream>>>(PS, PQ, 1792, 32, 229376.0, depthnorm_g, depthnorm_b, BN2);
-  k_mfma_nt<96,0><<<224, 256, 0, stream>>>(XP, W2H, W2L, CSTp, ZRES,
+  k_mfma_nt<96,0><<<224, 256, 0, stream>>>(XP, nullptr, nullptr, W2H, W2L, CSTp, ZRES,
       nullptr, nullptr, nullptr, nullptr);
-  k_att<<<3584, 256, 0, stream>>>(Z1, ZG, BN2, U, tf_fc_b, ATTp);
+  k_att<<<3584, 256, 0, stream>>>(Z1, ZG, BN2, U, tf_fc_b, ATTp, RS, RQ);
   k_tf<<<1, 1024, 0, stream>>>(ATTp, tf_norm_g, tf_norm_b, tf_conv_w, tf_conv_b, tf_fc_b, A1p, A2p);
-  k_statsA<<<3584, 256, 0, stream>>>(Z1, ZG, BN2, A1p, RS, RQ);
-  k_bnfin_rows<<<7, 256, 0, stream>>>(RS, RQ, 7, BD, 1048576.0, dctnorm_g, dctnorm_b, BN3);
+  k_bnfin_scaled<<<7, 256, 0, stream>>>(RS, RQ, A1p, dctnorm_g, dctnorm_b, BN3);
   k_statsC<<<3584, 256, 0, stream>>>(Z1, ZG, BN2, A1p, BN3, dctconv_w, dctconv_b, RS, RQ);
   k_bnfin_rows<<<7, 256, 0, stream>>>(RS, RQ, 7, BD, 1048576.0, dctnorm_g, dctnorm_b, BN4);
-  k_final<<<3584, 256, 0, stream>>>(Z1, ZG, BN2, A1p, A2p, BN3, BN4, dctconv_w, dctconv_b, XP, RS, RQ);
+  k_final<<<3584, 256, 0, stream>>>(Z1, ZG, BN2, A1p, A2p, BN3, BN4, dctconv_w, dctconv_b,
+      ZFH, ZFL, RS, RQ);
   k_bnfin_rows<<<7, 256, 0, stream>>>(RS, RQ, 7, BD, 1048576.0, dctnorm_g, dctnorm_b, BN5);
-  k_mfma_nt<48,1><<<224, 256, 0, stream>>>(XP, W1H, W1L, mlp_b1, H2p,
+  k_mfma_nt<48,2><<<224, 256, 0, stream>>>(nullptr, ZFH, ZFL, W1H, W1L, mlp_b1, H2p,
       BN5, BN5+7, RS, RQ);
   k_bnfin_rows<<<7, 256, 0, stream>>>(RS, RQ, 7, BD, 98304.0, mlpnorm_g, mlpnorm_b, BN6);
   k_out<<<5376, 256, 0, stream>>>(H2p, BN6, mlp_w2, mlp_b2, ZRES, out);
```

After: 356.0 us. -6.3%, faster.
